# Performance work log

Hardware: AMD Instinct MI355X
Metric: run time of the kernel (lower is better)

The kernel has to match this reference:

```python
import jax, jax.numpy as jnp
import numpy as np

SQRT2 = float(np.sqrt(2.0))


def setup_inputs() -> dict:
    key = jax.random.key(0)
    B, C, M, N = 128, 1, 512, 512
    img = jax.random.normal(key, (B, C, M, N), dtype=jnp.float32)
    return {"img": img}


def reference(img) -> jnp.ndarray:
    # img: [B, C=1, M, N]. Output: [B, 1, P, Q] with P=M, Q=N.
    B, C, M, N = img.shape
    P, Q = M, N
    m = jnp.arange(M, dtype=jnp.float32)
    n = jnp.arange(N, dtype=jnp.float32)
    p = jnp.arange(P, dtype=jnp.float32)
    q = jnp.arange(Q, dtype=jnp.float32)
    # Original: u = pi*(2*grid_x+1)*grid_p/(2M) -> depends only on (q, n); note /(2M) as in source.
    Cq = jnp.cos(jnp.pi * (2.0 * n[None, :] + 1.0) * q[:, None] / (2.0 * M))  # [Q, N]
    # Original: v = pi*(2*grid_y+1)*grid_q/(2N) -> depends only on (p, m); note /(2N) as in source.
    Cp = jnp.cos(jnp.pi * (2.0 * m[None, :] + 1.0) * p[:, None] / (2.0 * N))  # [P, M]
    # a_p * a_q = 2/M everywhere (source uses M for both), with p==0 row and q==0 col each / sqrt(2).
    row = jnp.where(jnp.arange(P) == 0, 1.0 / SQRT2, 1.0)[:, None]
    col = jnp.where(jnp.arange(Q) == 0, 1.0 / SQRT2, 1.0)[None, :]
    scale = (2.0 / M) * row * col  # [P, Q]
    # Separable DCT: y[b,c,p,q] = scale[p,q] * sum_{m,n} img[b,c,m,n] * Cp[p,m] * Cq[q,n]
    y = jnp.einsum('bcmn,pm,qn->bcpq', img, Cp, Cq)
    return y * scale
```

## Files before the change

kernel.cpp:

```cpp
#include <hip/hip_runtime.h>


typedef unsigned short u16;
typedef __attribute__((ext_vector_type(8))) short short8;
typedef __attribute__((ext_vector_type(4))) float float4v;
typedef __attribute__((ext_vector_type(4))) unsigned short ushort4v;

typedef const __attribute__((address_space(1))) void* gptr_t;
typedef __attribute__((address_space(3))) void* lptr_t;

__device__ __forceinline__ u16 f2h(float f) {
  _Float16 h = (_Float16)f;
  return __builtin_bit_cast(u16, h);
}

__device__ __forceinline__ void gload16(const void* g, void* l) {
  __builtin_amdgcn_global_load_lds((gptr_t)g, (lptr_t)l, 16, 0, 0);
}

__global__ void dct_coeff_kernel(u16* __restrict__ ch) {
  int idx = blockIdx.x * blockDim.x + threadIdx.x;
  int k = idx >> 9, i = idx & 511;
  float a = 3.14159274101257324f * (float)(2 * i + 1);
  float arg = (a * (float)k) * (1.0f / 1024.0f);
  ch[idx] = f2h(cosf(arg));
}

template <int PASS>
__global__ __launch_bounds__(256, 3) void dct_gemm_kernel(
    const float* __restrict__ X,
    const u16* __restrict__ W,
    const u16* __restrict__ C,
    u16* __restrict__ Wout,
    float* __restrict__ Y) {
  __shared__ u16 lds[2][2][128 * 32];

  const int tid = threadIdx.x;
  const int w = tid >> 6;
  const int ln = tid & 63;
  const int ln15 = ln & 15;
  const int s0 = ln >> 4;
  const int virt = (blockIdx.x & 7) * 256 + (blockIdx.x >> 3);
  const int tile_n = virt & 3;
  const int tile_m = virt >> 2;
  const int row0 = tile_m * 128;
  const int n0 = tile_n * 128;
  const int wm = w >> 1, wn = w & 1;

  float4v acc[4][4];
#pragma unroll
  for (int i = 0; i < 4; ++i)
#pragma unroll
    for (int j = 0; j < 4; ++j) {
      float4v z = {0.f, 0.f, 0.f, 0.f};
      acc[i][j] = z;
    }

  auto stage_bf = [&](const u16* src, int gr0, int k0, u16* ldst) {
#pragma unroll
    for (int j2 = 0; j2 < 2; ++j2) {
      const int trow = w * 32 + j2 * 16 + (ln >> 2);
      const int sg = (ln & 3) ^ ((trow >> 1) & 3);
      const u16* g = src + (size_t)(gr0 + trow) * 512 + k0 + sg * 8;
      u16* l = ldst + (w * 32 + j2 * 16) * 32;
      gload16(g, l);
    }
  };

  auto stage_a1 = [&](int k0, u16* lh) {
#pragma unroll
    for (int j = 0; j < 4; ++j) {
      const int trow = w * 32 + j * 8 + (ln >> 3);
      const int s16 = ln & 7;
      const float4v v =
          *(const float4v*)(X + (size_t)(row0 + trow) * 512 + k0 + s16 * 4);
      ushort4v hh;
#pragma unroll
      for (int e = 0; e < 4; ++e) hh[e] = f2h(v[e]);
      const int off =
          trow * 32 + (((s16 >> 1) ^ ((trow >> 1) & 3)) << 3) + (s16 & 1) * 4;
      *(ushort4v*)(lh + off) = hh;
    }
  };

  auto stage_all = [&](int buf, int t) {
    const int k0 = t * 32;
    if constexpr (PASS == 1) {
      stage_a1(k0, lds[buf][0]);
    } else {
      stage_bf(W, row0, k0, lds[buf][0]);
    }
    stage_bf(C, n0, k0, lds[buf][1]);
  };

  auto compute = [&](int buf) {
    const u16* lA = lds[buf][0];
    const u16* lB = lds[buf][1];
    short8 a[4], b[4];
#pragma unroll
    for (int i = 0; i < 4; ++i) {
      const int ra = wm * 64 + i * 16 + ln15;
      const int oa = ra * 32 + ((s0 ^ ((ra >> 1) & 3)) << 3);
      a[i] = *(const short8*)(lA + oa);
      const int rb = wn * 64 + i * 16 + ln15;
      const int ob = rb * 32 + ((s0 ^ ((rb >> 1) & 3)) << 3);
      b[i] = *(const short8*)(lB + ob);
    }
#pragma unroll
    for (int i = 0; i < 4; ++i)
#pragma unroll
      for (int j = 0; j < 4; ++j)
        acc[i][j] =
            __builtin_amdgcn_mfma_f32_16x16x32_f16(a[i], b[j], acc[i][j], 0, 0, 0);
  };

  stage_all(0, 0);
  __syncthreads();
  for (int t = 0; t < 16; ++t) {
    const int cur = t & 1;
    if (t < 15) stage_all(cur ^ 1, t + 1);
    compute(cur);
    __syncthreads();
  }

  const float RS2 = 0.70710678118654752440f;
#pragma unroll
  for (int i = 0; i < 4; ++i) {
    const int il = wm * 64 + i * 16 + (ln >> 4) * 4;
    const int gi = row0 + il;
    const int b = gi >> 9;
    const int qm = gi & 511;
#pragma unroll
    for (int j = 0; j < 4; ++j) {
      const int jglob = n0 + wn * 64 + j * 16 + ln15;
      const size_t idx = (size_t)b * 262144 + (size_t)jglob * 512 + qm;
      const float4v v = acc[i][j];
      if constexpr (PASS == 1) {
        ushort4v h;
#pragma unroll
        for (int e = 0; e < 4; ++e) h[e] = f2h(v[e]);
        *(ushort4v*)(Wout + idx) = h;
      } else {
        const float sj = (jglob == 0) ? RS2 : 1.0f;
        const float sc = 0.00390625f * sj;
        float4v o;
#pragma unroll
        for (int e = 0; e < 4; ++e)
          o[e] = v[e] * sc * ((qm + e) == 0 ? RS2 : 1.0f);
        *(float4v*)(Y + idx) = o;
      }
    }
  }
}

extern "C" void kernel_launch(void* const* d_in, const int* in_sizes, int n_in,
                              void* d_out, int out_size, void* d_ws, size_t ws_size,
                              hipStream_t stream) {
  const float* img = (const float*)d_in[0];
  float* out = (float*)d_out;
  char* ws = (char*)d_ws;

  u16* Cf = (u16*)(ws);
  u16* W = (u16*)(ws + (1u << 20));

  dct_coeff_kernel<<<1024, 256, 0, stream>>>(Cf);
  dct_gemm_kernel<1><<<2048, 256, 0, stream>>>(img, nullptr, Cf, W, nullptr);
  dct_gemm_kernel<2><<<2048, 256, 0, stream>>>(nullptr, W, Cf, nullptr, out);
}
```

Before: 302.3 us.

## Use 256x256 tiles with triple-buffered async LDS staging and split-phase MFMA

Grows the block tile from 128x128 to 256x256, with 512 threads per block in a 2x4 wave grid. Staging moves to a 3-deep LDS ring filled with global_load_lds, guarded by manual vmcnt waits and raw barriers. In pass 1 the fp32 image is copied straight into LDS and converted to fp16 when fragments are read, replacing the register round-trip. Each k-step is split into two half-M MFMA phases that interleave prefetch and raise wave priority around the MFMAs. Intended gains are more data reuse per block and overlap of loads with compute, at the cost of more LDS and registers per block, fewer blocks, and fragile hand-tuned wait counts.

```diff
diff --git a/kernel.cpp b/kernel.cpp
--- a/kernel.cpp
+++ b/kernel.cpp
@@ -27,107 +27,164 @@
 }
 
 template <int PASS>
-__global__ __launch_bounds__(256, 3) void dct_gemm_kernel(
+__global__ __launch_bounds__(512, 2) void dct_gemm_kernel(
     const float* __restrict__ X,
     const u16* __restrict__ W,
     const u16* __restrict__ C,
     u16* __restrict__ Wout,
     float* __restrict__ Y) {
-  __shared__ u16 lds[2][2][128 * 32];
+  constexpr int ABYTES = (PASS == 1) ? (256 * 32 * 4) : (256 * 32 * 2);
+  constexpr int BBYTES = 256 * 32 * 2;
+  __shared__ __align__(1024) char lds_raw[3 * (ABYTES + BBYTES)];
 
   const int tid = threadIdx.x;
   const int w = tid >> 6;
   const int ln = tid & 63;
   const int ln15 = ln & 15;
   const int s0 = ln >> 4;
-  const int virt = (blockIdx.x & 7) * 256 + (blockIdx.x >> 3);
-  const int tile_n = virt & 3;
-  const int tile_m = virt >> 2;
-  const int row0 = tile_m * 128;
-  const int n0 = tile_n * 128;
-  const int wm = w >> 1, wn = w & 1;
-
-  float4v acc[4][4];
-#pragma unroll
-  for (int i = 0; i < 4; ++i)
+  const int virt = (blockIdx.x & 7) * 64 + (blockIdx.x >> 3);
+  const int tile_n = virt & 1;
+  const int tile_m = virt >> 1;
+  const int row0 = tile_m * 256;
+  const int n0 = tile_n * 256;
+  const int wm = w >> 2, wn = w & 3;
+
+  auto bufA32 = [&](int i) { return (float*)(lds_raw + i * (ABYTES + BBYTES)); };
+  auto bufA16 = [&](int i) { return (u16*)(lds_raw + i * (ABYTES + BBYTES)); };
+  auto bufB   = [&](int i) { return (u16*)(lds_raw + i * (ABYTES + BBYTES) + ABYTES); };
+
+  float4v acc[8][4];
+#pragma unroll
+  for (int i = 0; i < 8; ++i)
 #pragma unroll
     for (int j = 0; j < 4; ++j) {
       float4v z = {0.f, 0.f, 0.f, 0.f};
       acc[i][j] = z;
     }
 
-  auto stage_bf = [&](const u16* src, int gr0, int k0, u16* ldst) {
-#pragma unroll
-    for (int j2 = 0; j2 < 2; ++j2) {
-      const int trow = w * 32 + j2 * 16 + (ln >> 2);
-      const int sg = (ln & 3) ^ ((trow >> 1) & 3);
-      const u16* g = src + (size_t)(gr0 + trow) * 512 + k0 + sg * 8;
-      u16* l = ldst + (w * 32 + j2 * 16) * 32;
-      gload16(g, l);
-    }
-  };
-
-  auto stage_a1 = [&](int k0, u16* lh) {
+  auto stage_f16 = [&](const u16* src, int gr0, int k0, u16* dst, int seg) {
+    const int row = seg * 16 + (ln >> 2);
+    const int cg = (ln & 3) ^ ((row >> 1) & 3);
+    gload16(src + (size_t)(gr0 + row) * 512 + k0 + cg * 8, dst + seg * 512);
+  };
+  auto stage_f32 = [&](int k0, float* dst, int seg) {
+    const int row = seg * 8 + (ln >> 3);
+    const int cg = (ln & 7) ^ (row & 7);
+    gload16(X + (size_t)(row0 + row) * 512 + k0 + cg * 4, dst + seg * 256);
+  };
+
+  auto stage_phase = [&](int t, int ph) {
+    const int k0 = t * 32;
+    const int bi = t % 3;
+    if constexpr (PASS == 1) {
+      float* dA = bufA32(bi);
+      u16* dB = bufB(bi);
+      if (ph == 0) {
+        stage_f32(k0, dA, w * 4 + 0);
+        stage_f32(k0, dA, w * 4 + 1);
+        stage_f16(C, n0, k0, dB, w * 2 + 0);
+      } else {
+        stage_f32(k0, dA, w * 4 + 2);
+        stage_f32(k0, dA, w * 4 + 3);
+        stage_f16(C, n0, k0, dB, w * 2 + 1);
+      }
+    } else {
+      u16* dA = bufA16(bi);
+      u16* dB = bufB(bi);
+      if (ph == 0) {
+        stage_f16(W, row0, k0, dA, w * 2 + 0);
+        stage_f16(C, n0, k0, dB, w * 2 + 0);
+      } else {
+        stage_f16(W, row0, k0, dA, w * 2 + 1);
+        stage_f16(C, n0, k0, dB, w * 2 + 1);
+      }
+    }
+  };
+
+  auto load_B = [&](int t, short8* b) {
+    const u16* lB = bufB(t % 3);
 #pragma unroll
     for (int j = 0; j < 4; ++j) {
-      const int trow = w * 32 + j * 8 + (ln >> 3);
-      const int s16 = ln & 7;
-      const float4v v =
-          *(const float4v*)(X + (size_t)(row0 + trow) * 512 + k0 + s16 * 4);
-      ushort4v hh;
-#pragma unroll
-      for (int e = 0; e < 4; ++e) hh[e] = f2h(v[e]);
-      const int off =
-          trow * 32 + (((s16 >> 1) ^ ((trow >> 1) & 3)) << 3) + (s16 & 1) * 4;
-      *(ushort4v*)(lh + off) = hh;
-    }
-  };
-
-  auto stage_all = [&](int buf, int t) {
-    const int k0 = t * 32;
+      const int rb = wn * 64 + j * 16 + ln15;
+      const int ob = rb * 32 + ((s0 ^ ((rb >> 1) & 3)) << 3);
+      b[j] = *(const short8*)(lB + ob);
+    }
+  };
+
+  auto load_A_phase = [&](int t, int mh, short8* a) {
     if constexpr (PASS == 1) {
-      stage_a1(k0, lds[buf][0]);
+      const float* lA = bufA32(t % 3);
+#pragma unroll
+      for (int i = 0; i < 4; ++i) {
+        const int r = wm * 128 + mh * 64 + i * 16 + ln15;
+        const int m = r & 7;
+        const float4v f0 = *(const float4v*)(lA + r * 32 + (((2 * s0) ^ m) << 2));
+        const float4v f1 = *(const float4v*)(lA + r * 32 + ((((2 * s0) | 1) ^ m) << 2));
+        short8 v;
+#pragma unroll
+        for (int e = 0; e < 4; ++e) {
+          v[e] = (short)f2h(f0[e]);
+          v[4 + e] = (short)f2h(f1[e]);
+        }
+        a[i] = v;
+      }
     } else {
-      stage_bf(W, row0, k0, lds[buf][0]);
-    }
-    stage_bf(C, n0, k0, lds[buf][1]);
-  };
-
-  auto compute = [&](int buf) {
-    const u16* lA = lds[buf][0];
-    const u16* lB = lds[buf][1];
+      const u16* lA = bufA16(t % 3);
+#pragma unroll
+      for (int i = 0; i < 4; ++i) {
+        const int r = wm * 128 + mh * 64 + i * 16 + ln15;
+        const int o = r * 32 + ((s0 ^ ((r >> 1) & 3)) << 3);
+        a[i] = *(const short8*)(lA + o);
+      }
+    }
+  };
+
+  stage_phase(0, 0);
+  stage_phase(0, 1);
+  stage_phase(1, 0);
+  stage_phase(1, 1);
+
+#pragma unroll
+  for (int T = 0; T < 16; ++T) {
+    if (T < 15) {
+      if constexpr (PASS == 1)
+        asm volatile("s_waitcnt vmcnt(6)" ::: "memory");
+      else
+        asm volatile("s_waitcnt vmcnt(4)" ::: "memory");
+    } else {
+      asm volatile("s_waitcnt vmcnt(0)" ::: "memory");
+    }
+    asm volatile("s_barrier" ::: "memory");
+
     short8 a[4], b[4];
-#pragma unroll
-    for (int i = 0; i < 4; ++i) {
-      const int ra = wm * 64 + i * 16 + ln15;
-      const int oa = ra * 32 + ((s0 ^ ((ra >> 1) & 3)) << 3);
-      a[i] = *(const short8*)(lA + oa);
-      const int rb = wn * 64 + i * 16 + ln15;
-      const int ob = rb * 32 + ((s0 ^ ((rb >> 1) & 3)) << 3);
-      b[i] = *(const short8*)(lB + ob);
-    }
+    load_B(T, b);
+    load_A_phase(T, 0, a);
+    if (T < 14) stage_phase(T + 2, 0);
+    __builtin_amdgcn_s_setprio(1);
 #pragma unroll
     for (int i = 0; i < 4; ++i)
 #pragma unroll
       for (int j = 0; j < 4; ++j)
         acc[i][j] =
             __builtin_amdgcn_mfma_f32_16x16x32_f16(a[i], b[j], acc[i][j], 0, 0, 0);
-  };
-
-  stage_all(0, 0);
-  __syncthreads();
-  for (int t = 0; t < 16; ++t) {
-    const int cur = t & 1;
-    if (t < 15) stage_all(cur ^ 1, t + 1);
-    compute(cur);
-    __syncthreads();
+    __builtin_amdgcn_s_setprio(0);
+
+    load_A_phase(T, 1, a);
+    if (T < 14) stage_phase(T + 2, 1);
+    __builtin_amdgcn_s_setprio(1);
+#pragma unroll
+    for (int i = 0; i < 4; ++i)
+#pragma unroll
+      for (int j = 0; j < 4; ++j)
+        acc[4 + i][j] = __builtin_amdgcn_mfma_f32_16x16x32_f16(a[i], b[j],
+                                                               acc[4 + i][j], 0, 0, 0);
+    __builtin_amdgcn_s_setprio(0);
   }
 
   const float RS2 = 0.70710678118654752440f;
 #pragma unroll
-  for (int i = 0; i < 4; ++i) {
-    const int il = wm * 64 + i * 16 + (ln >> 4) * 4;
-    const int gi = row0 + il;
+  for (int i = 0; i < 8; ++i) {
+    const int gi = row0 + wm * 128 + i * 16 + (ln >> 4) * 4;
     const int b = gi >> 9;
     const int qm = gi & 511;
 #pragma unroll
@@ -161,9 +218,9 @@
   char* ws = (char*)d_ws;
 
   u16* Cf = (u16*)(ws);
-  u16* W = (u16*)(ws + (1u << 20));
+  u16* Wb = (u16*)(ws + (1u << 20));
 
   dct_coeff_kernel<<<1024, 256, 0, stream>>>(Cf);
-  dct_gemm_kernel<1><<<2048, 256, 0, stream>>>(img, nullptr, Cf, W, nullptr);
-  dct_gemm_kernel<2><<<2048, 256, 0, stream>>>(nullptr, W, Cf, nullptr, out);
-}
+  dct_gemm_kernel<1><<<512, 512, 0, stream>>>(img, nullptr, Cf, Wb, nullptr);
+  dct_gemm_kernel<2><<<512, 512, 0, stream>>>(nullptr, Wb, Cf, nullptr, out);
+}
```

New measurement: 289.9 us. 1.04x faster.
